# Kernel tuning notes

Measured on AMD Instinct MI355X. Metric: run time of the kernel, lower is better.

Reference implementation:

```python
import jax, jax.numpy as jnp
import numpy as np

N, D_IN, D_H = 8192, 512, 1024


def setup_inputs() -> dict:
    key = jax.random.key(0)
    ks = jax.random.split(key, 24)
    s = 0.02
    def W(k, o, i):
        return (jax.random.normal(k, (o, i), jnp.float32) * s)
    def b(k, o):
        return (jax.random.normal(k, (o,), jnp.float32) * s)
    inp = {}
    inp["event_times"] = jnp.sort(jax.random.uniform(ks[0], (N,), jnp.float32) * 100.0)
    inp["event_marks"] = jax.random.normal(ks[1], (N, D_IN), jnp.float32)
    inp["T"] = 100
    inp["Wp"] = W(ks[2], D_H, D_IN); inp["bp"] = b(ks[3], D_H)
    inp["Wi"] = W(ks[4], D_H, D_H); inp["bi"] = b(ks[5], D_H)
    inp["Wf"] = W(ks[6], D_H, D_H); inp["bf"] = b(ks[7], D_H)
    inp["Wo"] = W(ks[8], D_H, D_H); inp["bo"] = b(ks[9], D_H)
    inp["Wz"] = W(ks[10], D_H, D_H); inp["bz"] = b(ks[11], D_H)
    inp["Wd"] = W(ks[12], D_H, D_H); inp["bd"] = b(ks[13], D_H)
    inp["Ui"] = W(ks[14], D_H, D_H)
    inp["Uf"] = W(ks[15], D_H, D_H)
    inp["Uo"] = W(ks[16], D_H, D_H)
    inp["Uz"] = W(ks[17], D_H, D_H)
    inp["Ud"] = W(ks[18], D_H, D_H)
    return inp


def reference(event_times, event_marks, T, Wp, bp, Wi, bi, Wf, bf, Wo, bo, Wz, bz, Wd, bd, Ui, Uf, Uo, Uz, Ud):
    # Batched input-side GEMMs (x depends only on marks, not on recurrent state)
    X = event_marks @ Wp.T + bp                 # [N, H]
    gxi = X @ Wi.T + bi
    gxf = X @ Wf.T + bf
    gxo = X @ Wo.T + bo
    gxz = X @ Wz.T + bz
    gxd = X @ Wd.T + bd
    # dt[0] = 0: first step sees zero decay (prev_decay is zeros anyway)
    dts = jnp.concatenate([jnp.zeros((1,), X.dtype), jnp.diff(event_times)])

    def step(carry, inp):
        h, c, cb, pdec = carry
        xi, xf, xo, xz, xd, dt = inp
        # exponential cell decay toward c_bar since last event
        c = cb + (c - cb) * jnp.exp(-pdec * dt)
        ig = jax.nn.sigmoid(xi + h @ Ui.T)
        fg = jax.nn.sigmoid(xf + h @ Uf.T)
        og = jax.nn.sigmoid(xo + h @ Uo.T)
        z = jnp.tanh(xz + h @ Uz.T)
        c_new = fg * c + ig * z
        cb = fg * cb + ig * z
        dec = jax.nn.softplus(xd + h @ Ud.T)
        h = og * jnp.tanh(c_new)
        return (h, c_new, cb, dec), (h, c_new, dec)

    z0 = jnp.zeros((D_H,), X.dtype)
    (_, _, cb_final, _), (H, C, Dec) = jax.lax.scan(
        step, (z0, z0, z0, z0), (gxi, gxf, gxo, gxz, gxd, dts))
    return H, C, Dec, cb_final
```

## Files before the change

### kernel.cpp

```cpp
#include <hip/hip_runtime.h>
#include <hip/hip_bf16.h>
#include <stdint.h>

#define NSTEPS 8192
#define DH 1024
#define DIN 512
#define G5 5120
#define NHOUT ((size_t)NSTEPS * DH)

#define NBLK 128
#define DPB 8
#define WROWS 40
#define THREADS 320

typedef __attribute__((ext_vector_type(8))) __bf16 bf16x8;
typedef __attribute__((ext_vector_type(4))) float f32x4;
typedef __attribute__((ext_vector_type(4))) unsigned int u32x4;
typedef __attribute__((ext_vector_type(2))) unsigned int u32x2;

#if __has_builtin(__builtin_amdgcn_fdot2_f32_bf16)
#define HAVE_DOT2 1
typedef __attribute__((ext_vector_type(2))) short s16x2;
__device__ __forceinline__ s16x2 asp(unsigned int u) {
  union { unsigned int i; s16x2 s; } v;
  v.i = u;
  return v.s;
}
#else
#define HAVE_DOT2 0
#endif

__device__ __forceinline__ float bfbits2f(unsigned int u) {
  union { unsigned int i; float f; } v;
  v.i = u << 16;
  return v.f;
}
__device__ __forceinline__ float bfhi2f(unsigned int u) {
  union { unsigned int i; float f; } v;
  v.i = u & 0xffff0000u;
  return v.f;
}
__device__ __forceinline__ unsigned short f2bfbits(float f) {
  union { __bf16 b; unsigned short u; } v;
  v.b = (__bf16)f;
  return v.u;
}

__global__ void cvt_f32_bf16(const float* __restrict__ src,
                             unsigned short* __restrict__ dst, int n4) {
  int i = blockIdx.x * blockDim.x + threadIdx.x;
  int stride = gridDim.x * blockDim.x;
  for (; i < n4; i += stride) {
    float4 v = ((const float4*)src)[i];
    ushort4 o;
    o.x = f2bfbits(v.x);
    o.y = f2bfbits(v.y);
    o.z = f2bfbits(v.z);
    o.w = f2bfbits(v.w);
    ((ushort4*)dst)[i] = o;
  }
}

#define BM 128
#define BN 128
#define BK 32
#define PSTR 40

__global__ __launch_bounds__(256) void gemm_bt(
    const unsigned short* __restrict__ A,
    const unsigned short* __restrict__ Bt,
    const float* __restrict__ bias,
    unsigned short* __restrict__ C,
    int M, int N, int K, int permute) {
  __shared__ unsigned short As[BM * PSTR];
  __shared__ unsigned short Bs[BM * PSTR];
  const int tid = threadIdx.x;
  const int nbn = N / BN;
  const int m0 = (blockIdx.x / nbn) * BM;
  const int n0 = (blockIdx.x % nbn) * BN;
  const int w = tid >> 6;
  const int l = tid & 63;
  const int ln = l & 15;
  const int k8 = l >> 4;
  const int wr = (w >> 1) * 64;
  const int wc = (w & 1) * 64;
  const int row_a = tid >> 2;
  const int c8 = (tid & 3) * 8;

  f32x4 acc[4][4];
#pragma unroll
  for (int a = 0; a < 4; a++)
#pragma unroll
    for (int b = 0; b < 4; b++) acc[a][b] = f32x4{0.f, 0.f, 0.f, 0.f};

  for (int k0 = 0; k0 < K; k0 += BK) {
    uint4 a0 = *(const uint4*)(A + (size_t)(m0 + row_a) * K + k0 + c8);
    uint4 a1 = *(const uint4*)(A + (size_t)(m0 + row_a + 64) * K + k0 + c8);
    uint4 b0 = *(const uint4*)(Bt + (size_t)(n0 + row_a) * K + k0 + c8);
    uint4 b1 = *(const uint4*)(Bt + (size_t)(n0 + row_a + 64) * K + k0 + c8);
    __syncthreads();
    *(uint4*)(As + row_a * PSTR + c8) = a0;
    *(uint4*)(As + (row_a + 64) * PSTR + c8) = a1;
    *(uint4*)(Bs + row_a * PSTR + c8) = b0;
    *(uint4*)(Bs + (row_a + 64) * PSTR + c8) = b1;
    __syncthreads();
    bf16x8 af[4], bfr[4];
#pragma unroll
    for (int mi = 0; mi < 4; mi++)
      af[mi] = *(const bf16x8*)(As + (wr + mi * 16 + ln) * PSTR + k8 * 8);
#pragma unroll
    for (int ni = 0; ni < 4; ni++)
      bfr[ni] = *(const bf16x8*)(Bs + (wc + ni * 16 + ln) * PSTR + k8 * 8);
#pragma unroll
    for (int mi = 0; mi < 4; mi++)
#pragma unroll
      for (int ni = 0; ni < 4; ni++)
        acc[mi][ni] = __builtin_amdgcn_mfma_f32_16x16x32_bf16(
            af[mi], bfr[ni], acc[mi][ni], 0, 0, 0);
  }
#pragma unroll
  for (int ni = 0; ni < 4; ni++) {
    int n = n0 + wc + ni * 16 + ln;
    float bv = bias[n];
#pragma unroll
    for (int mi = 0; mi < 4; mi++) {
#pragma unroll
      for (int r = 0; r < 4; r++) {
        int m = m0 + wr + mi * 16 + k8 * 4 + r;
        size_t ci;
        if (permute) {
          unsigned j = (unsigned)n & 1023u;
          ci = (size_t)m * N +
               (size_t)((j >> 3) * 40u + (((unsigned)n >> 10) << 3) + (j & 7u));
        } else {
          ci = (size_t)m * N + n;
        }
        C[ci] = f2bfbits(acc[mi][ni][r] + bv);
      }
    }
  }
}

__global__ __launch_bounds__(THREADS) void scan_kernel(
    const float* __restrict__ times,
    const float* __restrict__ Ui, const float* __restrict__ Uf2,
    const float* __restrict__ Uo, const float* __restrict__ Uz,
    const float* __restrict__ Ud,
    const unsigned short* __restrict__ gxp,
    unsigned int* __restrict__ hbuf,
    float* __restrict__ out) {
  __shared__ u32x4 w2[16 * WROWS * 8];
#if HAVE_DOT2
  __shared__ unsigned int hpk[DH / 2];
#else
  __shared__ float hf[DH];
#endif
  __shared__ float s_lds[WROWS];

  const int tid = threadIdx.x;
  const int bid = blockIdx.x;
  const int j0 = bid * DPB;

  {
    const float* Us[5] = {Ui, Uf2, Uo, Uz, Ud};
    for (int idx = tid; idx < WROWS * 256; idx += THREADS) {
      int row = idx >> 8;
      int c4 = idx & 255;
      const float* src =
          Us[row >> 3] + (size_t)(j0 + (row & 7)) * DH + c4 * 4;
      float4 v = *(const float4*)src;
      ushort4 o;
      o.x = f2bfbits(v.x);
      o.y = f2bfbits(v.y);
      o.z = f2bfbits(v.z);
      o.w = f2bfbits(v.w);
      int i16 = c4 >> 4;
      int ln = (c4 & 15) >> 1;
      int half = c4 & 1;
      *(ushort4*)((char*)(w2 + (i16 * WROWS + row) * 8 + ln) + half * 8) = o;
    }
  }
#if HAVE_DOT2
  for (int k = tid; k < DH / 2; k += THREADS) hpk[k] = 0u;
#else
  for (int k = tid; k < DH; k += THREADS) hf[k] = 0.f;
#endif
  float c = 0.f, cbv = 0.f, cd_reg = 0.f;
  __syncthreads();

  const int row = tid >> 3;
  const int ln8 = tid & 7;
  const u32x4* w2p = w2 + row * 8 + ln8;

  for (int t = 0; t < NSTEPS; ++t) {
    float gval = 0.f;
    float tcur = 0.f;
    if (tid < WROWS)
      gval = bfbits2f((unsigned int)gxp[(size_t)t * G5 + bid * WROWS + tid]);
    if (tid < DPB) tcur = times[t];

    if (t > 0 && tid < 64) {
      const unsigned int want = (unsigned int)t;
      const u32x4* pb = (const u32x4*)(hbuf + ((t - 1) & 1) * DH) + tid;
      u32x4 A, B, C2, D2;
      for (;;) {
        asm volatile(
            "global_load_dwordx4 %0, %4, off sc1\n\t"
            "global_load_dwordx4 %1, %4, off offset:1024 sc1\n\t"
            "global_load_dwordx4 %2, %4, off offset:2048 sc1\n\t"
            "global_load_dwordx4 %3, %4, off offset:3072 sc1\n\t"
            "s_waitcnt vmcnt(0)"
            : "=&v"(A), "=&v"(B), "=&v"(C2), "=&v"(D2)
            : "v"(pb)
            : "memory");
        bool ok = (A[0] >> 16) == want && (A[1] >> 16) == want &&
                  (A[2] >> 16) == want && (A[3] >> 16) == want &&
                  (B[0] >> 16) == want && (B[1] >> 16) == want &&
                  (B[2] >> 16) == want && (B[3] >> 16) == want &&
                  (C2[0] >> 16) == want && (C2[1] >> 16) == want &&
                  (C2[2] >> 16) == want && (C2[3] >> 16) == want &&
                  (D2[0] >> 16) == want && (D2[1] >> 16) == want &&
                  (D2[2] >> 16) == want && (D2[3] >> 16) == want;
        if (__all(ok)) break;
      }
#if HAVE_DOT2
      u32x2 pA = {(A[0] & 0xffffu) | (A[1] << 16),
                  (A[2] & 0xffffu) | (A[3] << 16)};
      u32x2 pB = {(B[0] & 0xffffu) | (B[1] << 16),
                  (B[2] & 0xffffu) | (B[3] << 16)};
      u32x2 pC = {(C2[0] & 0xffffu) | (C2[1] << 16),
                  (C2[2] & 0xffffu) | (C2[3] << 16)};
      u32x2 pD = {(D2[0] & 0xffffu) | (D2[1] << 16),
                  (D2[2] & 0xffffu) | (D2[3] << 16)};
      *(u32x2*)(hpk + 2 * tid) = pA;
      *(u32x2*)(hpk + 128 + 2 * tid) = pB;
      *(u32x2*)(hpk + 256 + 2 * tid) = pC;
      *(u32x2*)(hpk + 384 + 2 * tid) = pD;
#else
      f32x4 o0 = {bfbits2f(A[0] & 0xffffu), bfbits2f(A[1] & 0xffffu),
                  bfbits2f(A[2] & 0xffffu), bfbits2f(A[3] & 0xffffu)};
      f32x4 o1 = {bfbits2f(B[0] & 0xffffu), bfbits2f(B[1] & 0xffffu),
                  bfbits2f(B[2] & 0xffffu), bfbits2f(B[3] & 0xffffu)};
      f32x4 o2 = {bfbits2f(C2[0] & 0xffffu), bfbits2f(C2[1] & 0xffffu),
                  bfbits2f(C2[2] & 0xffffu), bfbits2f(C2[3] & 0xffffu)};
      f32x4 o3 = {bfbits2f(D2[0] & 0xffffu), bfbits2f(D2[1] & 0xffffu),
                  bfbits2f(D2[2] & 0xffffu), bfbits2f(D2[3] & 0xffffu)};
      *(f32x4*)(hf + 0 + 4 * tid) = o0;
      *(f32x4*)(hf + 256 + 4 * tid) = o1;
      *(f32x4*)(hf + 512 + 4 * tid) = o2;
      *(f32x4*)(hf + 768 + 4 * tid) = o3;
#endif
    }
    __syncthreads();

    {
#if HAVE_DOT2
      float a0 = 0.f, a1 = 0.f, a2 = 0.f, a3 = 0.f;
#pragma unroll
      for (int i = 0; i < 16; i++) {
        u32x4 wv = w2p[i * WROWS * 8];
        u32x4 hv = *(const u32x4*)(hpk + i * 32 + ln8 * 4);
        a0 = __builtin_amdgcn_fdot2_f32_bf16(asp(wv[0]), asp(hv[0]), a0, false);
        a1 = __builtin_amdgcn_fdot2_f32_bf16(asp(wv[1]), asp(hv[1]), a1, false);
        a2 = __builtin_amdgcn_fdot2_f32_bf16(asp(wv[2]), asp(hv[2]), a2, false);
        a3 = __builtin_amdgcn_fdot2_f32_bf16(asp(wv[3]), asp(hv[3]), a3, false);
      }
      float s = (a0 + a1) + (a2 + a3);
#else
      float a0 = 0.f, a1 = 0.f;
#pragma unroll
      for (int i = 0; i < 16; i++) {
        u32x4 wv = w2p[i * WROWS * 8];
        const float* hp = hf + i * 64 + ln8 * 8;
        f32x4 h0 = *(const f32x4*)hp;
        f32x4 h1 = *(const f32x4*)(hp + 4);
        a0 += bfbits2f(wv[0] & 0xffffu) * h0[0];
        a1 += bfhi2f(wv[0]) * h0[1];
        a0 += bfbits2f(wv[1] & 0xffffu) * h0[2];
        a1 += bfhi2f(wv[1]) * h0[3];
        a0 += bfbits2f(wv[2] & 0xffffu) * h1[0];
        a1 += bfhi2f(wv[2]) * h1[1];
        a0 += bfbits2f(wv[3] & 0xffffu) * h1[2];
        a1 += bfhi2f(wv[3]) * h1[3];
      }
      float s = a0 + a1;
#endif
      s += __shfl_xor(s, 1);
      s += __shfl_xor(s, 2);
      s += __shfl_xor(s, 4);
      if (ln8 == 0) s_lds[row] = s;
    }
    __syncthreads();

    if (tid < 64) {
      const int d = tid & 7;
      float xi = __shfl(gval, d);
      float xf2 = __shfl(gval, 8 + d);
      float xo = __shfl(gval, 16 + d);
      float xz = __shfl(gval, 24 + d);
      float xd = __shfl(gval, 32 + d);
      unsigned int word = 0;
      float h = 0.f, cn = 0.f, ig = 0.f, fg = 0.f, z = 0.f, adv = 0.f;
      if (tid < DPB) {
        float si = s_lds[tid];
        float sf = s_lds[8 + tid];
        float so = s_lds[16 + tid];
        float sz = s_lds[24 + tid];
        float sd = s_lds[32 + tid];
        ig = 1.f / (1.f + __expf(-(xi + si)));
        fg = 1.f / (1.f + __expf(-(xf2 + sf)));
        float og = 1.f / (1.f + __expf(-(xo + so)));
        z = 1.f - 2.f / (__expf(2.f * (xz + sz)) + 1.f);
        cn = fg * cd_reg + ig * z;
        float th = 1.f - 2.f / (__expf(2.f * cn) + 1.f);
        h = og * th;
        adv = xd + sd;
        word =
            (((unsigned int)(t + 1) & 0xffffu) << 16) | (unsigned int)f2bfbits(h);
      }
      u32x4 pubv = {__shfl(word, 4 * tid + 0), __shfl(word, 4 * tid + 1),
                    __shfl(word, 4 * tid + 2), __shfl(word, 4 * tid + 3)};
      if (tid < 2) {
        u32x4* dst = (u32x4*)(hbuf + (t & 1) * DH + bid * DPB) + tid;
        asm volatile("global_store_dwordx4 %0, %1, off sc1" ::"v"(dst),
                     "v"(pubv)
                     : "memory");
      }
      if (tid < DPB) {
        float dec = fmaxf(adv, 0.f) + __logf(1.f + __expf(-fabsf(adv)));
        cbv = fg * cbv + ig * z;
        c = cn;
        int j = j0 + tid;
        out[(size_t)t * DH + j] = h;
        out[NHOUT + (size_t)t * DH + j] = cn;
        out[2 * NHOUT + (size_t)t * DH + j] = dec;
        float tn = times[t + (t < NSTEPS - 1 ? 1 : 0)];
        cd_reg = cbv + (cn - cbv) * __expf(-dec * (tn - tcur));
      }
    }
  }
  if (tid < DPB) out[3 * NHOUT + j0 + tid] = cbv;
}

extern "C" void kernel_launch(void* const* d_in, const int* in_sizes, int n_in,
                              void* d_out, int out_size, void* d_ws,
                              size_t ws_size, hipStream_t stream) {
  (void)in_sizes; (void)n_in; (void)out_size; (void)ws_size;
  const float* times = (const float*)d_in[0];
  const float* marks = (const float*)d_in[1];
  const float* Wp = (const float*)d_in[3];
  const float* bp = (const float*)d_in[4];
  const float* Wi = (const float*)d_in[5];
  const float* bi = (const float*)d_in[6];
  const float* Wf = (const float*)d_in[7];
  const float* bf_ = (const float*)d_in[8];
  const float* Wo = (const float*)d_in[9];
  const float* bo = (const float*)d_in[10];
  const float* Wz = (const float*)d_in[11];
  const float* bz = (const float*)d_in[12];
  const float* Wd = (const float*)d_in[13];
  const float* bd = (const float*)d_in[14];
  const float* Ui = (const float*)d_in[15];
  const float* Uf2 = (const float*)d_in[16];
  const float* Uo = (const float*)d_in[17];
  const float* Uz = (const float*)d_in[18];
  const float* Ud = (const float*)d_in[19];

  char* ws = (char*)d_ws;
  size_t off = 0;
  auto alloc = [&](size_t bytes) -> void* {
    void* p = ws + off;
    off += (bytes + 255) & ~(size_t)255;
    return p;
  };
  unsigned short* marks_bf = (unsigned short*)alloc((size_t)NSTEPS * DIN * 2);
  unsigned short* X_bf = (unsigned short*)alloc((size_t)NSTEPS * DH * 2);
  unsigned short* Wp_bf = (unsigned short*)alloc((size_t)DH * DIN * 2);
  unsigned short* W5_bf = (unsigned short*)alloc((size_t)G5 * DH * 2);
  float* bcat = (float*)alloc((size_t)G5 * 4);
  unsigned short* gxp = (unsigned short*)alloc((size_t)NSTEPS * G5 * 2);
  unsigned int* hbuf = (unsigned int*)alloc((size_t)2 * DH * 4);

  auto cvt = [&](const float* s, unsigned short* d, int n) {
    int n4 = n / 4;
    int grid = (n4 + 255) / 256;
    if (grid > 2048) grid = 2048;
    cvt_f32_bf16<<<grid, 256, 0, stream>>>(s, d, n4);
  };
  cvt(marks, marks_bf, NSTEPS * DIN);
  cvt(Wp, Wp_bf, DH * DIN);
  cvt(Wi, W5_bf + (size_t)0 * DH * DH, DH * DH);
  cvt(Wf, W5_bf + (size_t)1 * DH * DH, DH * DH);
  cvt(Wo, W5_bf + (size_t)2 * DH * DH, DH * DH);
  cvt(Wz, W5_bf + (size_t)3 * DH * DH, DH * DH);
  cvt(Wd, W5_bf + (size_t)4 * DH * DH, DH * DH);
  hipMemcpyAsync(bcat + 0 * DH, bi, DH * sizeof(float),
                 hipMemcpyDeviceToDevice, stream);
  hipMemcpyAsync(bcat + 1 * DH, bf_, DH * sizeof(float),
                 hipMemcpyDeviceToDevice, stream);
  hipMemcpyAsync(bcat + 2 * DH, bo, DH * sizeof(float),
                 hipMemcpyDeviceToDevice, stream);
  hipMemcpyAsync(bcat + 3 * DH, bz, DH * sizeof(float),
                 hipMemcpyDeviceToDevice, stream);
  hipMemcpyAsync(bcat + 4 * DH, bd, DH * sizeof(float),
                 hipMemcpyDeviceToDevice, stream);

  gemm_bt<<<(NSTEPS / BM) * (DH / BN), 256, 0, stream>>>(
      marks_bf, Wp_bf, bp, X_bf, NSTEPS, DH, DIN, 0);
  gemm_bt<<<(NSTEPS / BM) * (G5 / BN), 256, 0, stream>>>(
      X_bf, W5_bf, bcat, gxp, NSTEPS, G5, DH, 1);

  scan_kernel<<<NBLK, THREADS, 0, stream>>>(times, Ui, Uf2, Uo, Uz, Ud, gxp,
                                            hbuf, (float*)d_out);
}
```

Before: 14.58 ms.

## Move gate-input loads and output stores off the recurrent critical path

The second wave now loads the per-step gate inputs into LDS, and the time stamps are cached in LDS once at kernel start. The h/c/decay outputs of step t are staged in LDS and written to global memory by another wave during step t+1. Only the 8 threads that update the state now run the nonlinear gate math, and they no longer issue global loads or stores. The intent is to shorten the serial per-step latency, at the cost of extra LDS space and a one-step delay on output writes, which needs an epilogue for the final step.

```diff
diff --git a/kernel.cpp b/kernel.cpp
--- a/kernel.cpp
+++ b/kernel.cpp
@@ -156,6 +156,9 @@
   __shared__ float hf[DH];
 #endif
   __shared__ float s_lds[WROWS];
+  __shared__ float gx_lds[WROWS];
+  __shared__ float ostage[3 * DPB];
+  __shared__ float t_lds[NSTEPS];
 
   const int tid = threadIdx.x;
   const int bid = blockIdx.x;
@@ -180,24 +183,25 @@
       *(ushort4*)((char*)(w2 + (i16 * WROWS + row) * 8 + ln) + half * 8) = o;
     }
   }
+  for (int k = tid; k < NSTEPS / 4; k += THREADS)
+    ((float4*)t_lds)[k] = ((const float4*)times)[k];
 #if HAVE_DOT2
   for (int k = tid; k < DH / 2; k += THREADS) hpk[k] = 0u;
 #else
   for (int k = tid; k < DH; k += THREADS) hf[k] = 0.f;
 #endif
-  float c = 0.f, cbv = 0.f, cd_reg = 0.f;
+  float cbv = 0.f, cd_reg = 0.f;
   __syncthreads();
 
   const int row = tid >> 3;
   const int ln8 = tid & 7;
   const u32x4* w2p = w2 + row * 8 + ln8;
+  const int l1 = tid - 64;
 
   for (int t = 0; t < NSTEPS; ++t) {
-    float gval = 0.f;
-    float tcur = 0.f;
-    if (tid < WROWS)
-      gval = bfbits2f((unsigned int)gxp[(size_t)t * G5 + bid * WROWS + tid]);
-    if (tid < DPB) tcur = times[t];
+    unsigned short graw = 0;
+    if (l1 >= 0 && l1 < WROWS)
+      graw = gxp[(size_t)t * G5 + bid * WROWS + l1];
 
     if (t > 0 && tid < 64) {
       const unsigned int want = (unsigned int)t;
@@ -253,6 +257,11 @@
     }
     __syncthreads();
 
+    if (l1 >= 0 && l1 < WROWS)
+      gx_lds[l1] = bfbits2f((unsigned int)graw);
+    float oval = 0.f;
+    if (l1 >= 0 && l1 < 3 * DPB && t > 0) oval = ostage[l1];
+
     {
 #if HAVE_DOT2
       float a0 = 0.f, a1 = 0.f, a2 = 0.f, a3 = 0.f;
@@ -290,54 +299,59 @@
       s += __shfl_xor(s, 4);
       if (ln8 == 0) s_lds[row] = s;
     }
+    if (l1 >= 0 && l1 < 3 * DPB && t > 0) {
+      int g = l1 >> 3;
+      int d = l1 & 7;
+      out[(size_t)g * NHOUT + (size_t)(t - 1) * DH + j0 + d] = oval;
+    }
     __syncthreads();
 
-    if (tid < 64) {
-      const int d = tid & 7;
-      float xi = __shfl(gval, d);
-      float xf2 = __shfl(gval, 8 + d);
-      float xo = __shfl(gval, 16 + d);
-      float xz = __shfl(gval, 24 + d);
-      float xd = __shfl(gval, 32 + d);
-      unsigned int word = 0;
-      float h = 0.f, cn = 0.f, ig = 0.f, fg = 0.f, z = 0.f, adv = 0.f;
-      if (tid < DPB) {
-        float si = s_lds[tid];
-        float sf = s_lds[8 + tid];
-        float so = s_lds[16 + tid];
-        float sz = s_lds[24 + tid];
-        float sd = s_lds[32 + tid];
-        ig = 1.f / (1.f + __expf(-(xi + si)));
-        fg = 1.f / (1.f + __expf(-(xf2 + sf)));
-        float og = 1.f / (1.f + __expf(-(xo + so)));
-        z = 1.f - 2.f / (__expf(2.f * (xz + sz)) + 1.f);
-        cn = fg * cd_reg + ig * z;
-        float th = 1.f - 2.f / (__expf(2.f * cn) + 1.f);
-        h = og * th;
-        adv = xd + sd;
-        word =
-            (((unsigned int)(t + 1) & 0xffffu) << 16) | (unsigned int)f2bfbits(h);
-      }
-      u32x4 pubv = {__shfl(word, 4 * tid + 0), __shfl(word, 4 * tid + 1),
-                    __shfl(word, 4 * tid + 2), __shfl(word, 4 * tid + 3)};
+    if (tid < DPB) {
+      float si = s_lds[tid] + gx_lds[tid];
+      float sf = s_lds[8 + tid] + gx_lds[8 + tid];
+      float so = s_lds[16 + tid] + gx_lds[16 + tid];
+      float sz = s_lds[24 + tid] + gx_lds[24 + tid];
+      float ig = 1.f / (1.f + __expf(-si));
+      float fg = 1.f / (1.f + __expf(-sf));
+      float og = 1.f / (1.f + __expf(-so));
+      float z = 1.f - 2.f / (__expf(2.f * sz) + 1.f);
+      float cn = fg * cd_reg + ig * z;
+      float th = 1.f - 2.f / (__expf(2.f * cn) + 1.f);
+      float h = og * th;
+      unsigned int word =
+          (((unsigned int)(t + 1) & 0xffffu) << 16) | (unsigned int)f2bfbits(h);
+      u32x4 pubv;
+      pubv[0] = __shfl(word, 4 * tid + 0);
+      pubv[1] = __shfl(word, 4 * tid + 1);
+      pubv[2] = __shfl(word, 4 * tid + 2);
+      pubv[3] = __shfl(word, 4 * tid + 3);
       if (tid < 2) {
         u32x4* dst = (u32x4*)(hbuf + (t & 1) * DH + bid * DPB) + tid;
         asm volatile("global_store_dwordx4 %0, %1, off sc1" ::"v"(dst),
                      "v"(pubv)
                      : "memory");
       }
-      if (tid < DPB) {
-        float dec = fmaxf(adv, 0.f) + __logf(1.f + __expf(-fabsf(adv)));
-        cbv = fg * cbv + ig * z;
-        c = cn;
-        int j = j0 + tid;
-        out[(size_t)t * DH + j] = h;
-        out[NHOUT + (size_t)t * DH + j] = cn;
-        out[2 * NHOUT + (size_t)t * DH + j] = dec;
-        float tn = times[t + (t < NSTEPS - 1 ? 1 : 0)];
-        cd_reg = cbv + (cn - cbv) * __expf(-dec * (tn - tcur));
-      }
-    }
+      float sd = s_lds[32 + tid] + gx_lds[32 + tid];
+      float dec = fmaxf(sd, 0.f) + __logf(1.f + __expf(-fabsf(sd)));
+      cbv = fg * cbv + ig * z;
+      float tn = t_lds[t + (t < NSTEPS - 1 ? 1 : 0)];
+      float tc = t_lds[t];
+      cd_reg = cbv + (cn - cbv) * __expf(-dec * (tn - tc));
+      ostage[tid] = h;
+      ostage[8 + tid] = cn;
+      ostage[16 + tid] = dec;
+    } else if (tid >= 8 && tid < 64) {
+      unsigned int word = 0;
+      u32x4 pubv;
+      pubv[0] = __shfl(word, 4 * tid + 0);
+      (void)pubv;
+    }
+  }
+  __syncthreads();
+  if (l1 >= 0 && l1 < 3 * DPB) {
+    int g = l1 >> 3;
+    int d = l1 & 7;
+    out[(size_t)g * NHOUT + (size_t)(NSTEPS - 1) * DH + j0 + d] = ostage[l1];
   }
   if (tid < DPB) out[3 * NHOUT + j0 + tid] = cbv;
 }
```

Result: slower. 17.50 ms (+20.0%).
